# Performance work log

Measured on AMD Instinct MI355X. Metric: run time of the kernel, lower is better.

The kernel has to match this reference:

```python
import jax, jax.numpy as jnp
import numpy as np

HEAD_DIM = 64

def rotate_half(x):
    x1, x2 = jnp.split(x, 2, axis=-1)
    return jnp.concatenate([-x2, x1], axis=-1)

def setup_inputs() -> dict:
    key = jax.random.key(0)
    ks = jax.random.split(key, 6)
    B, T, E = 1, 2048, 2048
    H, KV, D = 32, 8, HEAD_DIM
    BS, W = 64, 256
    hidden_states = jax.random.normal(ks[0], (B, T, E), jnp.float32)
    Wq = jax.random.normal(ks[1], (H * D, E), jnp.float32) / np.float32(np.sqrt(E))
    Wk = jax.random.normal(ks[2], (KV * D, E), jnp.float32) / np.float32(np.sqrt(E))
    Wv = jax.random.normal(ks[3], (KV * D, E), jnp.float32) / np.float32(np.sqrt(E))
    Wo = jax.random.normal(ks[4], (E, H * D), jnp.float32) / np.float32(np.sqrt(H * D))
    # RoPE tables (Llama-style, theta=10000)
    pos = jnp.arange(T, dtype=jnp.float32)
    inv_freq = 1.0 / (10000.0 ** (jnp.arange(0, D, 2, dtype=jnp.float32) / D))
    freqs = pos[:, None] * inv_freq[None, :]                 # [T, D/2]
    emb = jnp.concatenate([freqs, freqs], axis=-1)           # [T, D]
    cos = jnp.cos(emb)[None]                                 # [1, T, D]
    sin = jnp.sin(emb)[None]
    rw_allow_blocks = jax.random.bernoulli(ks[5], 0.15, (B, T // BS, T // BS))
    return {"hidden_states": hidden_states, "cos": cos, "sin": sin,
            "Wq": Wq, "Wk": Wk, "Wv": Wv, "Wo": Wo,
            "rw_allow_blocks": rw_allow_blocks,
            "rw_block_size": BS, "rw_window_tokens": W}

def reference(hidden_states, cos, sin, Wq, Wk, Wv, Wo,
              rw_allow_blocks, rw_block_size, rw_window_tokens):
    B, T, E = hidden_states.shape
    D = HEAD_DIM
    H = Wq.shape[0] // D
    KV = Wk.shape[0] // D
    n_rep = H // KV  # num_key_value_groups
    scaling = D ** -0.5

    # projections -> [B, heads, T, D]
    q = (hidden_states @ Wq.T).reshape(B, T, H, D).transpose(0, 2, 1, 3)
    k = (hidden_states @ Wk.T).reshape(B, T, KV, D).transpose(0, 2, 1, 3)
    v = (hidden_states @ Wv.T).reshape(B, T, KV, D).transpose(0, 2, 1, 3)

    # rotary embedding (unsqueeze_dim=1)
    c = cos[:, None, :, :]
    s = sin[:, None, :, :]
    q = q * c + rotate_half(q) * s
    k = k * c + rotate_half(k) * s

    # repeat_kv for GQA
    k = jnp.repeat(k, n_rep, axis=1)
    v = jnp.repeat(v, n_rep, axis=1)

    scores = jnp.einsum('bhqd,bhkd->bhqk', q, k) * scaling   # [B,H,T,T]

    # expand block allow pattern to token resolution
    allow = jnp.repeat(jnp.repeat(rw_allow_blocks, rw_block_size, axis=1),
                       rw_block_size, axis=2)[:, :T, :T]     # [B,T,T]
    # causal sliding window + attention sink (first window tokens always visible)
    qi = jnp.arange(T)[:, None]
    ki = jnp.arange(T)[None, :]
    win = ((ki <= qi) & (ki >= qi - rw_window_tokens + 1)) | (ki < rw_window_tokens)
    allow = allow | win[None]

    neg = jnp.finfo(scores.dtype).min
    scores = jnp.where(allow[:, None, :, :], scores, neg)
    probs = jax.nn.softmax(scores.astype(jnp.float32), axis=-1).astype(q.dtype)

    out = jnp.einsum('bhqk,bhkd->bhqd', probs, v)            # [B,H,T,D]
    out = out.transpose(0, 2, 1, 3).reshape(B, T, H * D)
    return out @ Wo.T                                        # [B,T,E]
```

## Files before the change

### kernel.cpp

```cpp
#include <hip/hip_runtime.h>

typedef unsigned short bfu;
typedef __attribute__((ext_vector_type(8))) short short8;
typedef __attribute__((ext_vector_type(4))) float f32x4;

#define TT 2048
#define EE 2048

#define GBAR() do { __builtin_amdgcn_sched_barrier(0); \
                    __builtin_amdgcn_s_barrier();      \
                    __builtin_amdgcn_sched_barrier(0); } while (0)

__device__ __forceinline__ unsigned short f2bf(float f) {
  union { float fv; unsigned int u; } v; v.fv = f;
  unsigned int r = v.u + 0x7fffu + ((v.u >> 16) & 1u);
  return (unsigned short)(r >> 16);
}

__device__ __forceinline__ unsigned int cvtpk(float lo, float hi) {
  unsigned int r;
  asm("v_cvt_pk_bf16_f32 %0, %1, %2" : "=v"(r) : "v"(lo), "v"(hi));
  return r;
}

__device__ __forceinline__ void gload16(const void* g, void* l) {
  __builtin_amdgcn_global_load_lds(
      (const __attribute__((address_space(1))) unsigned int*)g,
      (__attribute__((address_space(3))) unsigned int*)l, 16, 0, 0);
}

__global__ __launch_bounds__(256) void cvt5(
    const float* __restrict__ s0, const float* __restrict__ s1,
    const float* __restrict__ s2, const float* __restrict__ s3,
    const float* __restrict__ s4,
    bfu* __restrict__ d0, bfu* __restrict__ d1, bfu* __restrict__ d2,
    bfu* __restrict__ d3, bfu* __restrict__ d4,
    const unsigned char* __restrict__ mask_in, unsigned char* __restrict__ mask_out) {
  if (blockIdx.y == 5) {
    if (blockIdx.x != 0) return;
    __shared__ int mis;
    if (threadIdx.x == 0) mis = 0;
    __syncthreads();
    int any = 0;
    for (int i = threadIdx.x; i < 1024; i += 256)
      if ((i & 3) != 0 && mask_in[i] != 0) any = 1;
    if (any) atomicAdd(&mis, 1);
    __syncthreads();
    for (int i = threadIdx.x; i < 1024; i += 256) {
      if (mis == 0) mask_out[i] = (((const int*)mask_in)[i] != 0) ? 1 : 0;
      else          mask_out[i] = mask_in[i] ? 1 : 0;
    }
    return;
  }
  const float* s; bfu* d; int n;
  switch (blockIdx.y) {
    case 0:  s = s0; d = d0; n = 4194304; break;
    case 1:  s = s1; d = d1; n = 4194304; break;
    case 2:  s = s2; d = d2; n = 1048576; break;
    case 3:  s = s3; d = d3; n = 1048576; break;
    default: s = s4; d = d4; n = 4194304; break;
  }
  for (int i = (blockIdx.x * 256 + threadIdx.x) * 8; i < n; i += 512 * 256 * 8) {
    float4 a = *(const float4*)(s + i);
    float4 b = *(const float4*)(s + i + 4);
    short8 pk;
    pk[0] = (short)f2bf(a.x); pk[1] = (short)f2bf(a.y);
    pk[2] = (short)f2bf(a.z); pk[3] = (short)f2bf(a.w);
    pk[4] = (short)f2bf(b.x); pk[5] = (short)f2bf(b.y);
    pk[6] = (short)f2bf(b.z); pk[7] = (short)f2bf(b.w);
    *(short8*)(d + i) = pk;
  }
}

__global__ __launch_bounds__(256) void gemm_qkv(
    const bfu* __restrict__ A, const bfu* __restrict__ Bq,
    const bfu* __restrict__ Bk, const bfu* __restrict__ Bv,
    bfu* __restrict__ qr, bfu* __restrict__ kro, bfu* __restrict__ vt,
    const float* __restrict__ cosb, const float* __restrict__ sinb, float qsc) {
  __shared__ bfu As[2][64 * 64];
  __shared__ bfu Bs[2][128 * 64];
  const int bx = blockIdx.x;
  int path, n0;
  const bfu* B;
  if (bx < 16)      { path = 0; B = Bq; n0 = bx * 128; }
  else if (bx < 20) { path = 1; B = Bk; n0 = (bx - 16) * 128; }
  else              { path = 2; B = Bv; n0 = (bx - 20) * 128; }
  const int t = threadIdx.x;
  const int wid = t >> 6, lane = t & 63;
  const int wr = wid >> 1, wc = wid & 1;
  const int lr = lane & 15, lh = lane >> 4;
  const int m0 = blockIdx.y * 64;
  const int K = EE;
  f32x4 acc[2][4] = {};

  auto stage = [&](int buf, int k0) {
    #pragma unroll
    for (int p = 0; p < 2; ++p) {
      int c = p * 256 + wid * 64 + lane;
      int row = c >> 3, s = c & 7;
      gload16(A + (size_t)(m0 + row) * K + k0 + ((s ^ (row & 7)) * 8),
              &As[buf][(p * 256 + wid * 64) * 8]);
    }
    #pragma unroll
    for (int p = 0; p < 4; ++p) {
      int c = p * 256 + wid * 64 + lane;
      int row = c >> 3, s = c & 7;
      gload16(B + (size_t)(n0 + row) * K + k0 + ((s ^ (row & 7)) * 8),
              &Bs[buf][(p * 256 + wid * 64) * 8]);
    }
  };

  stage(0, 0);
  for (int kt = 0; kt < 32; ++kt) {
    const int cur = kt & 1;
    if (kt < 31) {
      stage(cur ^ 1, (kt + 1) * 64);
      asm volatile("s_waitcnt vmcnt(6)" ::: "memory");
    } else {
      asm volatile("s_waitcnt vmcnt(0)" ::: "memory");
    }
    GBAR();
    #pragma unroll
    for (int ks = 0; ks < 2; ++ks) {
      short8 a[2], b[4];
      #pragma unroll
      for (int m = 0; m < 2; ++m)
        a[m] = *(const short8*)(&As[cur][(wr * 32 + m * 16 + lr) * 64 +
                                         (((ks * 4 + lh) ^ (lr & 7)) * 8)]);
      #pragma unroll
      for (int n = 0; n < 4; ++n)
        b[n] = *(const short8*)(&Bs[cur][(wc * 64 + n * 16 + lr) * 64 +
                                         (((ks * 4 + lh) ^ (lr & 7)) * 8)]);
      #pragma unroll
      for (int m = 0; m < 2; ++m)
        #pragma unroll
        for (int n = 0; n < 4; ++n)
          acc[m][n] = __builtin_amdgcn_mfma_f32_16x16x32_bf16(a[m], b[n], acc[m][n], 0, 0, 0);
    }
    GBAR();
  }
  #pragma unroll
  for (int m = 0; m < 2; ++m)
    #pragma unroll
    for (int r = 0; r < 4; ++r) {
      const int row = m0 + wr * 32 + m * 16 + lh * 4 + r;
      #pragma unroll
      for (int n = 0; n < 4; ++n) {
        const int col = n0 + wc * 64 + n * 16 + lr;
        float x = acc[m][n][r];
        if (path == 2) {
          vt[((size_t)(row >> 6) * 512 + col) * 64 + (row & 63)] = f2bf(x);
        } else {
          const int d = col & 63;
          float xp = (n < 2) ? -acc[m][n + 2][r] : acc[m][n - 2][r];
          float c = cosb[row * 64 + d], s = sinb[row * 64 + d];
          float sc = (path == 0) ? qsc : 1.0f;
          bfu* dst = (path == 0) ? qr : kro;
          dst[((size_t)(col >> 6) * TT + row) * 64 + d] = f2bf((x * c + xp * s) * sc);
        }
      }
    }
}

__global__ __launch_bounds__(256) void gemm_o(
    const bfu* __restrict__ A, const bfu* __restrict__ B,
    float* __restrict__ outF, int M, int N, int K) {
  __shared__ bfu As[2][64 * 64];
  __shared__ bfu Bs[2][128 * 64];
  const int t = threadIdx.x;
  const int wid = t >> 6, lane = t & 63;
  const int wr = wid >> 1, wc = wid & 1;
  const int lr = lane & 15, lh = lane >> 4;
  const int m0 = blockIdx.y * 64, n0 = blockIdx.x * 128;
  f32x4 acc[2][4] = {};

  auto stage = [&](int buf, int k0) {
    #pragma unroll
    for (int p = 0; p < 2; ++p) {
      int c = p * 256 + wid * 64 + lane;
      int row = c >> 3, s = c & 7;
      gload16(A + (size_t)(m0 + row) * K + k0 + ((s ^ (row & 7)) * 8),
              &As[buf][(p * 256 + wid * 64) * 8]);
    }
    #pragma unroll
    for (int p = 0; p < 4; ++p) {
      int c = p * 256 + wid * 64 + lane;
      int row = c >> 3, s = c & 7;
      gload16(B + (size_t)(n0 + row) * K + k0 + ((s ^ (row & 7)) * 8),
              &Bs[buf][(p * 256 + wid * 64) * 8]);
    }
  };

  stage(0, 0);
  const int nk = K >> 6;
  for (int kt = 0; kt < nk; ++kt) {
    const int cur = kt & 1;
    if (kt < nk - 1) {
      stage(cur ^ 1, (kt + 1) * 64);
      asm volatile("s_waitcnt vmcnt(6)" ::: "memory");
    } else {
      asm volatile("s_waitcnt vmcnt(0)" ::: "memory");
    }
    GBAR();
    #pragma unroll
    for (int ks = 0; ks < 2; ++ks) {
      short8 a[2], b[4];
      #pragma unroll
      for (int m = 0; m < 2; ++m)
        a[m] = *(const short8*)(&As[cur][(wr * 32 + m * 16 + lr) * 64 +
                                         (((ks * 4 + lh) ^ (lr & 7)) * 8)]);
      #pragma unroll
      for (int n = 0; n < 4; ++n)
        b[n] = *(const short8*)(&Bs[cur][(wc * 64 + n * 16 + lr) * 64 +
                                         (((ks * 4 + lh) ^ (lr & 7)) * 8)]);
      #pragma unroll
      for (int m = 0; m < 2; ++m)
        #pragma unroll
        for (int n = 0; n < 4; ++n)
          acc[m][n] = __builtin_amdgcn_mfma_f32_16x16x32_bf16(a[m], b[n], acc[m][n], 0, 0, 0);
    }
    GBAR();
  }
  #pragma unroll
  for (int m = 0; m < 2; ++m)
    #pragma unroll
    for (int r = 0; r < 4; ++r) {
      const int row = m0 + wr * 32 + m * 16 + lh * 4 + r;
      #pragma unroll
      for (int n = 0; n < 4; ++n)
        outF[(size_t)row * N + n0 + wc * 64 + n * 16 + lr] = acc[m][n][r];
    }
}

__global__ __launch_bounds__(256, 4) void attn_kernel(
    const bfu* __restrict__ qr, const bfu* __restrict__ kr,
    const bfu* __restrict__ vt, const unsigned char* __restrict__ allow,
    bfu* __restrict__ ao) {
  const int qb = blockIdx.x, h = blockIdx.y, kv = h >> 2;
  const int t = threadIdx.x, wid = t >> 6, lane = t & 63;
  const int lr = lane & 15, lh = lane >> 4;
  const int q0 = qb * 64;
  const int qrow = q0 + wid * 16 + lr;
  __shared__ bfu KB[2][64 * 64];
  __shared__ bfu VB[2][64 * 64];
  __shared__ bfu P[4][16 * 64];
  bfu* Pw = P[wid];

  unsigned int amask = 0, emask = 0;
  for (int kb = 0; kb < 32; ++kb) {
    bool bm = allow[qb * 32 + kb] != 0;
    bool fw = (kb < 4) || (kb >= qb - 3 && kb <= qb - 1);
    bool ed = (kb == qb) || (kb == qb - 4);
    if (bm || fw || ed) {
      amask |= 1u << kb;
      if (!bm && !fw) emask |= 1u << kb;
    }
  }

  short8 bq[2];
  #pragma unroll
  for (int ks = 0; ks < 2; ++ks)
    bq[ks] = *(const short8*)(qr + ((size_t)h * TT + qrow) * 64 + ks * 32 + lh * 8);

  f32x4 o[4] = {};
  float m_reg = -1e30f, l_reg = 0.f;

  auto stage = [&](bfu* buf, const bfu* gbase) {
    #pragma unroll
    for (int c = 0; c < 2; ++c) {
      int chunk = wid * 128 + c * 64 + lane;
      int row = chunk >> 3, s = chunk & 7;
      gload16(gbase + row * 64 + (s ^ (row & 7)) * 8,
              buf + (wid * 128 + c * 64) * 8);
    }
  };

  auto qk_tile = [&](const bfu* KBuf, int kb, f32x4 s[4]) {
    __builtin_amdgcn_s_setprio(1);
    #pragma unroll
    for (int j = 0; j < 4; ++j) {
      const int row = j * 16 + lr;
      short8 a0 = *(const short8*)(KBuf + row * 64 + ((lh    ) ^ (row & 7)) * 8);
      short8 a1 = *(const short8*)(KBuf + row * 64 + ((lh + 4) ^ (row & 7)) * 8);
      f32x4 z = {};
      z = __builtin_amdgcn_mfma_f32_16x16x32_bf16(a0, bq[0], z, 0, 0, 0);
      s[j] = __builtin_amdgcn_mfma_f32_16x16x32_bf16(a1, bq[1], z, 0, 0, 0);
    }
    __builtin_amdgcn_s_setprio(0);
    if ((emask >> kb) & 1) {
      #pragma unroll
      for (int j = 0; j < 4; ++j)
        #pragma unroll
        for (int reg = 0; reg < 4; ++reg) {
          int k = kb * 64 + j * 16 + lh * 4 + reg;
          bool ok = (k <= qrow && k >= qrow - 255) || (k < 256);
          if (!ok) s[j][reg] = -1e30f;
        }
    }
  };

  auto pv_tile = [&](const bfu* VBuf, f32x4 s[4]) {
    #pragma unroll
    for (int j = 0; j < 4; ++j) {
      unsigned int w0 = cvtpk(s[j][0], s[j][1]);
      unsigned int w1 = cvtpk(s[j][2], s[j][3]);
      int base = lr * 64 + (((j * 2 + (lh >> 1)) ^ (lr & 7)) * 8) + (lh & 1) * 4;
      *(unsigned int*)(Pw + base) = w0;
      *(unsigned int*)(Pw + base + 2) = w1;
    }
    short8 pa[2];
    #pragma unroll
    for (int ks = 0; ks < 2; ++ks)
      pa[ks] = *(const short8*)(Pw + lr * 64 + (((ks * 4 + lh) ^ (lr & 7)) * 8));
    __builtin_amdgcn_s_setprio(1);
    #pragma unroll
    for (int n = 0; n < 4; ++n) {
      #pragma unroll
      for (int ks = 0; ks < 2; ++ks) {
        const int row = n * 16 + lr;
        short8 bv = *(const short8*)(VBuf + row * 64 + ((ks * 4 + lh) ^ (row & 7)) * 8);
        o[n] = __builtin_amdgcn_mfma_f32_16x16x32_bf16(pa[ks], bv, o[n], 0, 0, 0);
      }
    }
    __builtin_amdgcn_s_setprio(0);
  };

  unsigned int am = amask;
  while (am) {
    const int k1 = __ffs(am) - 1; am &= am - 1;
    int k2 = -1;
    if (am) { k2 = __ffs(am) - 1; am &= am - 1; }

    __syncthreads();
    stage(KB[0], kr + ((size_t)kv * TT + k1 * 64) * 64);
    stage(VB[0], vt + ((size_t)k1 * 512 + kv * 64) * 64);
    if (k2 >= 0) {
      stage(KB[1], kr + ((size_t)kv * TT + k2 * 64) * 64);
      stage(VB[1], vt + ((size_t)k2 * 512 + kv * 64) * 64);
    }
    __syncthreads();

    f32x4 s1[4], s2[4];
    qk_tile(KB[0], k1, s1);
    if (k2 >= 0) qk_tile(KB[1], k2, s2);

    float mx = fmaxf(fmaxf(s1[0][0], s1[0][1]), fmaxf(s1[0][2], s1[0][3]));
    #pragma unroll
    for (int j = 1; j < 4; ++j)
      mx = fmaxf(mx, fmaxf(fmaxf(s1[j][0], s1[j][1]), fmaxf(s1[j][2], s1[j][3])));
    if (k2 >= 0) {
      #pragma unroll
      for (int j = 0; j < 4; ++j)
        mx = fmaxf(mx, fmaxf(fmaxf(s2[j][0], s2[j][1]), fmaxf(s2[j][2], s2[j][3])));
    }
    mx = fmaxf(mx, __shfl_xor(mx, 16));
    mx = fmaxf(mx, __shfl_xor(mx, 32));

    if (__any(mx > m_reg)) {
      float mnew = fmaxf(m_reg, mx);
      float corr = exp2f(m_reg - mnew);
      m_reg = mnew;
      l_reg *= corr;
      #pragma unroll
      for (int r = 0; r < 4; ++r) {
        float cr = __shfl(corr, lh * 4 + r);
        #pragma unroll
        for (int n = 0; n < 4; ++n) o[n][r] *= cr;
      }
    }

    float rs = 0.f;
    #pragma unroll
    for (int j = 0; j < 4; ++j)
      #pragma unroll
      for (int reg = 0; reg < 4; ++reg) {
        float p = exp2f(s1[j][reg] - m_reg);
        s1[j][reg] = p;
        rs += p;
      }
    if (k2 >= 0) {
      #pragma unroll
      for (int j = 0; j < 4; ++j)
        #pragma unroll
        for (int reg = 0; reg < 4; ++reg) {
          float p = exp2f(s2[j][reg] - m_reg);
          s2[j][reg] = p;
          rs += p;
        }
    }
    rs += __shfl_xor(rs, 16);
    rs += __shfl_xor(rs, 32);
    l_reg += rs;

    pv_tile(VB[0], s1);
    if (k2 >= 0) pv_tile(VB[1], s2);
  }

  #pragma unroll
  for (int r = 0; r < 4; ++r) {
    float ln = __shfl(l_reg, lh * 4 + r);
    float inv = 1.0f / ln;
    #pragma unroll
    for (int n = 0; n < 4; ++n) {
      float val = o[n][r] * inv;
      ao[(size_t)(q0 + wid * 16 + lh * 4 + r) * EE + h * 64 + n * 16 + lr] = f2bf(val);
    }
  }
}

extern "C" void kernel_launch(void* const* d_in, const int* in_sizes, int n_in,
                              void* d_out, int out_size, void* d_ws, size_t ws_size,
                              hipStream_t stream) {
  const float* hs   = (const float*)d_in[0];
  const float* cosb = (const float*)d_in[1];
  const float* sinb = (const float*)d_in[2];
  const float* Wq   = (const float*)d_in[3];
  const float* Wk   = (const float*)d_in[4];
  const float* Wv   = (const float*)d_in[5];
  const float* Wo   = (const float*)d_in[6];
  const unsigned char* allow_raw = (const unsigned char*)d_in[7];
  float* out = (float*)d_out;

  char* ws = (char*)d_ws;
  const size_t MB = 1024 * 1024;
  bfu* hsb = (bfu*)(ws);
  bfu* wqb = (bfu*)(ws + 8 * MB);
  bfu* wkb = (bfu*)(ws + 16 * MB);
  bfu* wvb = (bfu*)(ws + 18 * MB);
  bfu* wob = (bfu*)(ws + 20 * MB);
  bfu* qr  = (bfu*)(ws + 28 * MB);
  bfu* kr  = (bfu*)(ws + 36 * MB);
  bfu* vt  = (bfu*)(ws + 38 * MB);
  unsigned char* maskc = (unsigned char*)(ws + 40 * MB);
  bfu* ao = hsb;

  cvt5<<<dim3(512, 6), 256, 0, stream>>>(hs, Wq, Wk, Wv, Wo,
                                         hsb, wqb, wkb, wvb, wob,
                                         allow_raw, maskc);

  const float QSC = 0.125f * 1.44269504088896f;
  gemm_qkv<<<dim3(24, 32), 256, 0, stream>>>(
      hsb, wqb, wkb, wvb, qr, kr, vt, cosb, sinb, QSC);

  attn_kernel<<<dim3(32, 32), 256, 0, stream>>>(qr, kr, vt, maskc, ao);

  gemm_o<<<dim3(16, 32), 256, 0, stream>>>(ao, wob, out, 2048, 2048, 2048);
}
```

Measured before the change: 134.6 us.

## Double-buffer K/V tile pairs in attention to overlap loads with compute

Doubles the LDS buffers for K and V so the next pair of allowed key blocks is prefetched asynchronously while the current pair is processed. Explicit vmcnt waits and barriers replace the previous pattern of loading everything and then syncing. Query blocks are also launched in reverse order so the heavier late blocks start first, and the occupancy hint in the launch bounds is removed. The larger LDS footprint lowers the number of resident workgroups per CU, trading occupancy for overlap.

```diff
diff --git a/kernel.cpp b/kernel.cpp
--- a/kernel.cpp
+++ b/kernel.cpp
@@ -232,17 +232,18 @@
     }
 }
 
-__global__ __launch_bounds__(256, 4) void attn_kernel(
+__global__ __launch_bounds__(256) void attn_kernel(
     const bfu* __restrict__ qr, const bfu* __restrict__ kr,
     const bfu* __restrict__ vt, const unsigned char* __restrict__ allow,
     bfu* __restrict__ ao) {
-  const int qb = blockIdx.x, h = blockIdx.y, kv = h >> 2;
+  const int qb = 31 - blockIdx.x;
+  const int h = blockIdx.y, kv = h >> 2;
   const int t = threadIdx.x, wid = t >> 6, lane = t & 63;
   const int lr = lane & 15, lh = lane >> 4;
   const int q0 = qb * 64;
   const int qrow = q0 + wid * 16 + lr;
-  __shared__ bfu KB[2][64 * 64];
-  __shared__ bfu VB[2][64 * 64];
+  __shared__ bfu KB[2][2][64 * 64];
+  __shared__ bfu VB[2][2][64 * 64];
   __shared__ bfu P[4][16 * 64];
   bfu* Pw = P[wid];
 
@@ -265,13 +266,17 @@
   f32x4 o[4] = {};
   float m_reg = -1e30f, l_reg = 0.f;
 
-  auto stage = [&](bfu* buf, const bfu* gbase) {
+  auto stage_tile = [&](int sp, int ti, int kb) {
+    const bfu* kg = kr + ((size_t)kv * TT + kb * 64) * 64;
+    const bfu* vg = vt + ((size_t)kb * 512 + kv * 64) * 64;
     #pragma unroll
     for (int c = 0; c < 2; ++c) {
       int chunk = wid * 128 + c * 64 + lane;
       int row = chunk >> 3, s = chunk & 7;
-      gload16(gbase + row * 64 + (s ^ (row & 7)) * 8,
-              buf + (wid * 128 + c * 64) * 8);
+      int goff = row * 64 + (s ^ (row & 7)) * 8;
+      int loff = (wid * 128 + c * 64) * 8;
+      gload16(kg + goff, &KB[sp][ti][loff]);
+      gload16(vg + goff, &VB[sp][ti][loff]);
     }
   };
 
@@ -326,23 +331,36 @@
   };
 
   unsigned int am = amask;
-  while (am) {
-    const int k1 = __ffs(am) - 1; am &= am - 1;
-    int k2 = -1;
-    if (am) { k2 = __ffs(am) - 1; am &= am - 1; }
-
-    __syncthreads();
-    stage(KB[0], kr + ((size_t)kv * TT + k1 * 64) * 64);
-    stage(VB[0], vt + ((size_t)k1 * 512 + kv * 64) * 64);
-    if (k2 >= 0) {
-      stage(KB[1], kr + ((size_t)kv * TT + k2 * 64) * 64);
-      stage(VB[1], vt + ((size_t)k2 * 512 + kv * 64) * 64);
-    }
-    __syncthreads();
+  int k1 = -1, k2 = -1;
+  if (am) { k1 = __ffs(am) - 1; am &= am - 1; }
+  if (am) { k2 = __ffs(am) - 1; am &= am - 1; }
+  int cur = 0;
+  if (k1 >= 0) {
+    stage_tile(0, 0, k1);
+    if (k2 >= 0) stage_tile(0, 1, k2);
+  }
+
+  while (k1 >= 0) {
+    int k3 = -1, k4 = -1;
+    if (am) { k3 = __ffs(am) - 1; am &= am - 1; }
+    if (am) { k4 = __ffs(am) - 1; am &= am - 1; }
+
+    if (k3 >= 0) {
+      stage_tile(cur ^ 1, 0, k3);
+      if (k4 >= 0) {
+        stage_tile(cur ^ 1, 1, k4);
+        asm volatile("s_waitcnt vmcnt(8)" ::: "memory");
+      } else {
+        asm volatile("s_waitcnt vmcnt(4)" ::: "memory");
+      }
+    } else {
+      asm volatile("s_waitcnt vmcnt(0)" ::: "memory");
+    }
+    GBAR();
 
     f32x4 s1[4], s2[4];
-    qk_tile(KB[0], k1, s1);
-    if (k2 >= 0) qk_tile(KB[1], k2, s2);
+    qk_tile(KB[cur][0], k1, s1);
+    if (k2 >= 0) qk_tile(KB[cur][1], k2, s2);
 
     float mx = fmaxf(fmaxf(s1[0][0], s1[0][1]), fmaxf(s1[0][2], s1[0][3]));
     #pragma unroll
@@ -392,8 +410,11 @@
     rs += __shfl_xor(rs, 32);
     l_reg += rs;
 
-    pv_tile(VB[0], s1);
-    if (k2 >= 0) pv_tile(VB[1], s2);
+    pv_tile(VB[cur][0], s1);
+    if (k2 >= 0) pv_tile(VB[cur][1], s2);
+
+    GBAR();
+    k1 = k3; k2 = k4; cur ^= 1;
   }
 
   #pragma unroll
```

New measurement: 145.6 us. +8.2%, slower.
